# Optimization experiments

Hardware: AMD Instinct MI355X
Metric: run time of the kernel (lower is better)

Reference implementation:

```python
import jax, jax.numpy as jnp
import numpy as np

N_EMB = 384
BLOCK = 128

def setup_inputs() -> dict:
    key = jax.random.key(0)
    k1, k2, k3, k4 = jax.random.split(key, 4)
    B, T, hs = 1024, 128, 64
    x = jax.random.normal(k1, (B, T, N_EMB), dtype=jnp.float32)
    Wk = jax.random.normal(k2, (hs, N_EMB), dtype=jnp.float32) * (N_EMB ** -0.5)
    Wq = jax.random.normal(k3, (hs, N_EMB), dtype=jnp.float32) * (N_EMB ** -0.5)
    Wv = jax.random.normal(k4, (hs, N_EMB), dtype=jnp.float32) * (N_EMB ** -0.5)
    return {"x": x, "Wk": Wk, "Wq": Wq, "Wv": Wv}

def reference(x, Wk, Wq, Wv):
    B, T, C = x.shape
    # nn.Linear(n_emb, head_size, bias=False): y = x @ W.T
    k = jnp.einsum('btc,hc->bth', x, Wk)  # [B,T,hs]
    q = jnp.einsum('btc,hc->bth', x, Wq)
    v = jnp.einsum('btc,hc->bth', x, Wv)
    # NOTE: source scales by C**-0.5 where C = n_emb (384), not head_size
    w = jnp.einsum('bth,bsh->bts', q, k) * (C ** -0.5)  # [B,T,T]
    causal = jnp.tril(jnp.ones((T, T), dtype=bool))
    w = jnp.where(causal, w, -jnp.inf)
    w = jax.nn.softmax(w, axis=-1)
    # dropout is identity in eval mode
    out = jnp.einsum('bts,bsh->bth', w, v)  # [B,T,hs]
    return out
```

## Files before the change

kernel.cpp:

```cpp
#include <hip/hip_runtime.h>

typedef __bf16 bf16_t;
typedef __attribute__((ext_vector_type(8))) __bf16 bf16x8;
typedef __attribute__((ext_vector_type(4))) float floatx4;

#define MFMA16(a, b, c) __builtin_amdgcn_mfma_f32_16x16x32_bf16((a), (b), (c), 0, 0, 0)

constexpr int TT = 128;
constexpr int CD = 384;
constexpr int HS = 64;
constexpr int BB = 1024;

constexpr int QK_STR = 72;
constexpr int VT_STR = 136;
constexpr int QS_OFF = 0;
constexpr int KS_OFF = TT * QK_STR;
constexpr int VT_OFF = 2 * TT * QK_STR;
constexpr int PS_OFF = 0;
constexpr int SMEM_N = 2 * TT * QK_STR + HS * VT_STR;

__global__ void wconv_kernel(const float* __restrict__ wq, const float* __restrict__ wk,
                             const float* __restrict__ wv, bf16_t* __restrict__ wf) {
    const int t = blockIdx.x * 256 + threadIdx.x;
    if (t >= 3 * 12 * 4 * 64) return;
    const int lane = t & 63;
    const int f    = t >> 6;
    const int nt   = f & 3;
    const int kki  = (f >> 2) % 12;
    const int proj = f / 48;
    const float* W = (proj == 0) ? wq : ((proj == 1) ? wk : wv);
    const int h = 16 * nt + (lane & 15);
    const int c = 32 * kki + 8 * (lane >> 4);
    const float* src = W + h * CD + c;
    bf16x8 o;
#pragma unroll
    for (int j = 0; j < 8; ++j) o[j] = (bf16_t)src[j];
    *(bf16x8*)(wf + (size_t)t * 8) = o;
}

__launch_bounds__(256, 2)
__global__ void attn_kernel(const float* __restrict__ x, const bf16_t* __restrict__ wf,
                            float* __restrict__ out) {
    __shared__ __align__(16) bf16_t smem[SMEM_N];
    const int b    = blockIdx.x;
    const int lane = threadIdx.x & 63;
    const int w    = threadIdx.x >> 6;
    const int l15  = lane & 15;
    const int g    = lane >> 4;
    const float* xb = x + (size_t)b * TT * CD;
    const bf16_t* wfl = wf + (size_t)lane * 8;

    floatx4 accq[2][4], acck[2][4], accv[2][4];
#pragma unroll
    for (int mt = 0; mt < 2; ++mt)
#pragma unroll
        for (int nt = 0; nt < 4; ++nt) {
            accq[mt][nt] = (floatx4)0.0f;
            acck[mt][nt] = (floatx4)0.0f;
            accv[mt][nt] = (floatx4)0.0f;
        }

    float4 xa0[2], xa1[2];
    bf16x8 wb[12];
#pragma unroll
    for (int mt = 0; mt < 2; ++mt) {
        const float* p = xb + (size_t)(32 * w + 16 * mt + l15) * CD + 8 * g;
        xa0[mt] = *(const float4*)p;
        xa1[mt] = *(const float4*)(p + 4);
    }
#pragma unroll
    for (int pn = 0; pn < 12; ++pn) {
        const int proj = pn >> 2, nt = pn & 3;
        wb[pn] = *(const bf16x8*)(wfl + (size_t)((proj * 12 + 0) * 4 + nt) * 512);
    }

#pragma unroll
    for (int kki = 0; kki < 12; ++kki) {
        float4 xn0[2], xn1[2];
        bf16x8 wn[12];
        if (kki < 11) {
            const int c = 32 * (kki + 1) + 8 * g;
#pragma unroll
            for (int mt = 0; mt < 2; ++mt) {
                const float* p = xb + (size_t)(32 * w + 16 * mt + l15) * CD + c;
                xn0[mt] = *(const float4*)p;
                xn1[mt] = *(const float4*)(p + 4);
            }
#pragma unroll
            for (int pn = 0; pn < 12; ++pn) {
                const int proj = pn >> 2, nt = pn & 3;
                wn[pn] = *(const bf16x8*)(wfl + (size_t)((proj * 12 + kki + 1) * 4 + nt) * 512);
            }
        }
        bf16x8 a[2];
#pragma unroll
        for (int mt = 0; mt < 2; ++mt) {
            bf16x8 t;
            t[0] = (bf16_t)xa0[mt].x; t[1] = (bf16_t)xa0[mt].y;
            t[2] = (bf16_t)xa0[mt].z; t[3] = (bf16_t)xa0[mt].w;
            t[4] = (bf16_t)xa1[mt].x; t[5] = (bf16_t)xa1[mt].y;
            t[6] = (bf16_t)xa1[mt].z; t[7] = (bf16_t)xa1[mt].w;
            a[mt] = t;
        }
#pragma unroll
        for (int nt = 0; nt < 4; ++nt) {
            accq[0][nt] = MFMA16(a[0], wb[0 + nt], accq[0][nt]);
            accq[1][nt] = MFMA16(a[1], wb[0 + nt], accq[1][nt]);
            acck[0][nt] = MFMA16(a[0], wb[4 + nt], acck[0][nt]);
            acck[1][nt] = MFMA16(a[1], wb[4 + nt], acck[1][nt]);
            accv[0][nt] = MFMA16(a[0], wb[8 + nt], accv[0][nt]);
            accv[1][nt] = MFMA16(a[1], wb[8 + nt], accv[1][nt]);
        }
        if (kki < 11) {
#pragma unroll
            for (int mt = 0; mt < 2; ++mt) { xa0[mt] = xn0[mt]; xa1[mt] = xn1[mt]; }
#pragma unroll
            for (int pn = 0; pn < 12; ++pn) wb[pn] = wn[pn];
        }
    }

#pragma unroll
    for (int mt = 0; mt < 2; ++mt)
#pragma unroll
        for (int nt = 0; nt < 4; ++nt) {
            const int t0 = 32 * w + 16 * mt + 4 * g;
            const int h  = 16 * nt + l15;
#pragma unroll
            for (int r = 0; r < 4; ++r) {
                smem[QS_OFF + (t0 + r) * QK_STR + h] = (bf16_t)accq[mt][nt][r];
                smem[KS_OFF + (t0 + r) * QK_STR + h] = (bf16_t)acck[mt][nt][r];
                smem[VT_OFF + h * VT_STR + t0 + r]   = (bf16_t)accv[mt][nt][r];
            }
        }
    __syncthreads();

    floatx4 sacc[2][8];
#pragma unroll
    for (int mt = 0; mt < 2; ++mt)
#pragma unroll
        for (int nt = 0; nt < 8; ++nt) sacc[mt][nt] = (floatx4)0.0f;

#pragma unroll
    for (int kt = 0; kt < 2; ++kt) {
        const int hh = 32 * kt + 8 * g;
        bf16x8 aq[2];
        aq[0] = *(const bf16x8*)(smem + QS_OFF + (32 * w + l15) * QK_STR + hh);
        aq[1] = *(const bf16x8*)(smem + QS_OFF + (32 * w + 16 + l15) * QK_STR + hh);
#pragma unroll
        for (int nt = 0; nt < 8; ++nt) {
            if (16 * nt <= 32 * w + 31) {
                bf16x8 bk = *(const bf16x8*)(smem + KS_OFF + (16 * nt + l15) * QK_STR + hh);
                if (16 * nt <= 32 * w + 15) sacc[0][nt] = MFMA16(aq[0], bk, sacc[0][nt]);
                sacc[1][nt] = MFMA16(aq[1], bk, sacc[1][nt]);
            }
        }
    }
    __syncthreads();

    const float scale = 0.05103103630798287f;
#pragma unroll
    for (int mt = 0; mt < 2; ++mt) {
#pragma unroll
        for (int r = 0; r < 4; ++r) {
            const int t = 32 * w + 16 * mt + 4 * g + r;
            float vals[8];
            float vmax = -__builtin_inff();
#pragma unroll
            for (int nt = 0; nt < 8; ++nt) {
                const int s = 16 * nt + l15;
                float v = (s <= t) ? sacc[mt][nt][r] * scale : -__builtin_inff();
                vals[nt] = v;
                vmax = fmaxf(vmax, v);
            }
            vmax = fmaxf(vmax, __shfl_xor(vmax, 1));
            vmax = fmaxf(vmax, __shfl_xor(vmax, 2));
            vmax = fmaxf(vmax, __shfl_xor(vmax, 4));
            vmax = fmaxf(vmax, __shfl_xor(vmax, 8));
            float sum = 0.0f;
#pragma unroll
            for (int nt = 0; nt < 8; ++nt) {
                float e = __expf(vals[nt] - vmax);
                vals[nt] = e;
                sum += e;
            }
            sum += __shfl_xor(sum, 1);
            sum += __shfl_xor(sum, 2);
            sum += __shfl_xor(sum, 4);
            sum += __shfl_xor(sum, 8);
            const float inv = 1.0f / sum;
#pragma unroll
            for (int nt = 0; nt < 8; ++nt)
                smem[PS_OFF + t * VT_STR + 16 * nt + l15] = (bf16_t)(vals[nt] * inv);
        }
    }

    floatx4 oacc[2][4];
#pragma unroll
    for (int mt = 0; mt < 2; ++mt)
#pragma unroll
        for (int nt = 0; nt < 4; ++nt) oacc[mt][nt] = (floatx4)0.0f;

    for (int st = 0; st <= w; ++st) {
        const int ss = 32 * st + 8 * g;
        bf16x8 ap0 = *(const bf16x8*)(smem + PS_OFF + (32 * w + l15) * VT_STR + ss);
        bf16x8 ap1 = *(const bf16x8*)(smem + PS_OFF + (32 * w + 16 + l15) * VT_STR + ss);
#pragma unroll
        for (int nt = 0; nt < 4; ++nt) {
            bf16x8 bv = *(const bf16x8*)(smem + VT_OFF + (16 * nt + l15) * VT_STR + ss);
            oacc[0][nt] = MFMA16(ap0, bv, oacc[0][nt]);
            oacc[1][nt] = MFMA16(ap1, bv, oacc[1][nt]);
        }
    }

    float* ob = out + (size_t)b * TT * HS;
#pragma unroll
    for (int mt = 0; mt < 2; ++mt)
#pragma unroll
        for (int nt = 0; nt < 4; ++nt) {
            const int t0 = 32 * w + 16 * mt + 4 * g;
            const int h  = 16 * nt + l15;
#pragma unroll
            for (int r = 0; r < 4; ++r)
                ob[(size_t)(t0 + r) * HS + h] = oacc[mt][nt][r];
        }
}

extern "C" void kernel_launch(void* const* d_in, const int* in_sizes, int n_in,
                              void* d_out, int out_size, void* d_ws, size_t ws_size,
                              hipStream_t stream) {
    const float* x  = (const float*)d_in[0];
    const float* wk = (const float*)d_in[1];
    const float* wq = (const float*)d_in[2];
    const float* wv = (const float*)d_in[3];
    float* out = (float*)d_out;

    bf16_t* wf = (bf16_t*)d_ws;

    wconv_kernel<<<36, 256, 0, stream>>>(wq, wk, wv, wf);
    attn_kernel<<<BB, 256, 0, stream>>>(x, wf, out);
}
```

Before: 329.2 us.

## Stage x and weight chunks into LDS via async global_load_lds double buffering

```diff
diff --git a/kernel.cpp b/kernel.cpp
--- a/kernel.cpp
+++ b/kernel.cpp
@@ -5,11 +5,18 @@
 typedef __attribute__((ext_vector_type(4))) float floatx4;
 
 #define MFMA16(a, b, c) __builtin_amdgcn_mfma_f32_16x16x32_bf16((a), (b), (c), 0, 0, 0)
+#define GLOAD_LDS(g, l)                                                                      \
+    __builtin_amdgcn_global_load_lds((const __attribute__((address_space(1))) unsigned int*)(g), \
+                                     (__attribute__((address_space(3))) unsigned int*)(l), 16, 0, 0)
 
 constexpr int TT = 128;
 constexpr int CD = 384;
 constexpr int HS = 64;
 constexpr int BB = 1024;
+constexpr int NCH = 12;
+
+constexpr int XB0 = 0, XB1 = 17408, WB0 = 34816, WB1 = 47104;
+constexpr int SMEM_BYTES = 59392;
 
 constexpr int QK_STR = 72;
 constexpr int VT_STR = 136;
@@ -17,17 +24,16 @@
 constexpr int KS_OFF = TT * QK_STR;
 constexpr int VT_OFF = 2 * TT * QK_STR;
 constexpr int PS_OFF = 0;
-constexpr int SMEM_N = 2 * TT * QK_STR + HS * VT_STR;
 
 __global__ void wconv_kernel(const float* __restrict__ wq, const float* __restrict__ wk,
                              const float* __restrict__ wv, bf16_t* __restrict__ wf) {
     const int t = blockIdx.x * 256 + threadIdx.x;
-    if (t >= 3 * 12 * 4 * 64) return;
+    if (t >= 144 * 64) return;
     const int lane = t & 63;
     const int f    = t >> 6;
     const int nt   = f & 3;
-    const int kki  = (f >> 2) % 12;
-    const int proj = f / 48;
+    const int proj = (f >> 2) % 3;
+    const int kki  = f / 12;
     const float* W = (proj == 0) ? wq : ((proj == 1) ? wk : wv);
     const int h = 16 * nt + (lane & 15);
     const int c = 32 * kki + 8 * (lane >> 4);
@@ -41,14 +47,40 @@
 __launch_bounds__(256, 2)
 __global__ void attn_kernel(const float* __restrict__ x, const bf16_t* __restrict__ wf,
                             float* __restrict__ out) {
-    __shared__ __align__(16) bf16_t smem[SMEM_N];
+    __shared__ __align__(16) char smem_raw[SMEM_BYTES];
+    bf16_t* smem = (bf16_t*)smem_raw;
     const int b    = blockIdx.x;
     const int lane = threadIdx.x & 63;
     const int w    = threadIdx.x >> 6;
     const int l15  = lane & 15;
     const int g    = lane >> 4;
-    const float* xb = x + (size_t)b * TT * CD;
-    const bf16_t* wfl = wf + (size_t)lane * 8;
+    const char* xb  = (const char*)(x + (size_t)b * TT * CD);
+    const char* wfb = (const char*)wf;
+
+    int      xi[5];
+    unsigned xg[5];
+#pragma unroll
+    for (int t2 = 0; t2 < 5; ++t2) {
+        const int i = w + 4 * t2;
+        xi[t2] = i;
+        unsigned u   = (unsigned)i * 1024u + (unsigned)lane * 16u;
+        unsigned p   = u / 272u;
+        unsigned rem = u - 272u * p;
+        unsigned row = 2u * p + (rem >> 7);
+        xg[t2] = (rem < 256u) ? row * (CD * 4u) + (rem & 127u) : 0u;
+    }
+
+    auto stage = [&](int c) {
+        const char* xsrc = xb + c * 128;
+        char*       xd   = smem_raw + ((c & 1) ? XB1 : XB0);
+#pragma unroll
+        for (int t2 = 0; t2 < 5; ++t2)
+            if (xi[t2] <= 16) GLOAD_LDS(xsrc + xg[t2], xd + xi[t2] * 1024);
+        const char* wsrc = wfb + (size_t)(c * 12 + 3 * w) * 1024 + (size_t)lane * 16;
+        char*       wd   = smem_raw + ((c & 1) ? WB1 : WB0) + 3 * w * 1024;
+#pragma unroll
+        for (int j = 0; j < 3; ++j) GLOAD_LDS(wsrc + (size_t)j * 1024, wd + j * 1024);
+    };
 
     floatx4 accq[2][4], acck[2][4], accv[2][4];
 #pragma unroll
@@ -60,63 +92,41 @@
             accv[mt][nt] = (floatx4)0.0f;
         }
 
-    float4 xa0[2], xa1[2];
-    bf16x8 wb[12];
-#pragma unroll
-    for (int mt = 0; mt < 2; ++mt) {
-        const float* p = xb + (size_t)(32 * w + 16 * mt + l15) * CD + 8 * g;
-        xa0[mt] = *(const float4*)p;
-        xa1[mt] = *(const float4*)(p + 4);
-    }
-#pragma unroll
-    for (int pn = 0; pn < 12; ++pn) {
-        const int proj = pn >> 2, nt = pn & 3;
-        wb[pn] = *(const bf16x8*)(wfl + (size_t)((proj * 12 + 0) * 4 + nt) * 512);
-    }
-
-#pragma unroll
-    for (int kki = 0; kki < 12; ++kki) {
-        float4 xn0[2], xn1[2];
-        bf16x8 wn[12];
-        if (kki < 11) {
-            const int c = 32 * (kki + 1) + 8 * g;
-#pragma unroll
-            for (int mt = 0; mt < 2; ++mt) {
-                const float* p = xb + (size_t)(32 * w + 16 * mt + l15) * CD + c;
-                xn0[mt] = *(const float4*)p;
-                xn1[mt] = *(const float4*)(p + 4);
-            }
-#pragma unroll
-            for (int pn = 0; pn < 12; ++pn) {
-                const int proj = pn >> 2, nt = pn & 3;
-                wn[pn] = *(const bf16x8*)(wfl + (size_t)((proj * 12 + kki + 1) * 4 + nt) * 512);
-            }
-        }
+    stage(0);
+    __syncthreads();
+
+    for (int c = 0; c < NCH; ++c) {
+        if (c + 1 < NCH) stage(c + 1);
+
+        const char*   xs = smem_raw + ((c & 1) ? XB1 : XB0);
+        const char*   ws = smem_raw + ((c & 1) ? WB1 : WB0);
+
         bf16x8 a[2];
 #pragma unroll
         for (int mt = 0; mt < 2; ++mt) {
+            const int   R = 32 * w + 16 * mt + l15;
+            const char* p = xs + (R >> 1) * 272 + (R & 1) * 128 + 32 * g;
+            float4 f0 = *(const float4*)p;
+            float4 f1 = *(const float4*)(p + 16);
             bf16x8 t;
-            t[0] = (bf16_t)xa0[mt].x; t[1] = (bf16_t)xa0[mt].y;
-            t[2] = (bf16_t)xa0[mt].z; t[3] = (bf16_t)xa0[mt].w;
-            t[4] = (bf16_t)xa1[mt].x; t[5] = (bf16_t)xa1[mt].y;
-            t[6] = (bf16_t)xa1[mt].z; t[7] = (bf16_t)xa1[mt].w;
+            t[0] = (bf16_t)f0.x; t[1] = (bf16_t)f0.y; t[2] = (bf16_t)f0.z; t[3] = (bf16_t)f0.w;
+            t[4] = (bf16_t)f1.x; t[5] = (bf16_t)f1.y; t[6] = (bf16_t)f1.z; t[7] = (bf16_t)f1.w;
             a[mt] = t;
         }
-#pragma unroll
-        for (int nt = 0; nt < 4; ++nt) {
-            accq[0][nt] = MFMA16(a[0], wb[0 + nt], accq[0][nt]);
-            accq[1][nt] = MFMA16(a[1], wb[0 + nt], accq[1][nt]);
-            acck[0][nt] = MFMA16(a[0], wb[4 + nt], acck[0][nt]);
-            acck[1][nt] = MFMA16(a[1], wb[4 + nt], acck[1][nt]);
-            accv[0][nt] = MFMA16(a[0], wb[8 + nt], accv[0][nt]);
-            accv[1][nt] = MFMA16(a[1], wb[8 + nt], accv[1][nt]);
-        }
-        if (kki < 11) {
-#pragma unroll
-            for (int mt = 0; mt < 2; ++mt) { xa0[mt] = xn0[mt]; xa1[mt] = xn1[mt]; }
-#pragma unroll
-            for (int pn = 0; pn < 12; ++pn) wb[pn] = wn[pn];
-        }
+        bf16x8 wbf[12];
+#pragma unroll
+        for (int pn = 0; pn < 12; ++pn)
+            wbf[pn] = *(const bf16x8*)(ws + pn * 1024 + lane * 16);
+#pragma unroll
+        for (int nt = 0; nt < 4; ++nt) {
+            accq[0][nt] = MFMA16(a[0], wbf[0 + nt], accq[0][nt]);
+            accq[1][nt] = MFMA16(a[1], wbf[0 + nt], accq[1][nt]);
+            acck[0][nt] = MFMA16(a[0], wbf[4 + nt], acck[0][nt]);
+            acck[1][nt] = MFMA16(a[1], wbf[4 + nt], acck[1][nt]);
+            accv[0][nt] = MFMA16(a[0], wbf[8 + nt], accv[0][nt]);
+            accv[1][nt] = MFMA16(a[1], wbf[8 + nt], accv[1][nt]);
+        }
+        __syncthreads();
     }
 
 #pragma unroll
```

Result: faster. 307.5 us (-6.6%).
